# Kernel optimization log

Hardware: AMD Instinct MI355X
Metric: run time of the kernel (lower is better)

Reference implementation:

```python
import jax, jax.numpy as jnp
from jax import lax
import numpy as np

TEMPERATURE = 0.8
TOP_K = 50
TOP_P = 0.9
REP_PENALTY = 1.2


def setup_inputs() -> dict:
    key = jax.random.key(0)
    k1, k2 = jax.random.split(key)
    B, V, T = 256, 50257, 2048
    logits = jax.random.normal(k1, (B, V), dtype=jnp.float32) * 4.0  # spread so top-p is non-trivial
    generated = jax.random.randint(k2, (B, T), 0, V, dtype=jnp.int64)
    return {"logits": logits, "generated": generated}


def reference(logits, generated):
    """One decode-step of LLM.generate: temperature -> repetition penalty ->
    top-k filter -> top-p (nucleus) filter -> softmax -> multinomial sample.
    Returns (next_token [B], probs [B, V])."""
    B, V = logits.shape
    x = logits / TEMPERATURE

    # repetition penalty: divide logits at every previously-generated token id
    rows = jnp.arange(B)[:, None]
    present = jnp.zeros((B, V), dtype=bool).at[rows, generated].set(True)
    x = jnp.where(present, x / REP_PENALTY, x)

    # top-k: mask everything strictly below the k-th largest logit
    kth = lax.top_k(x, TOP_K)[0][:, -1:]  # [B, 1]
    x = jnp.where(x < kth, -jnp.inf, x)

    # top-p: sort descending, softmax, cumsum, drop tail mass > p (always keep top-1)
    order = jnp.argsort(-x, axis=-1)                      # [B, V] descending order
    sorted_logits = jnp.take_along_axis(x, order, axis=-1)
    cum = jnp.cumsum(jax.nn.softmax(sorted_logits, axis=-1), axis=-1)
    remove_sorted = (cum > TOP_P).at[:, 0].set(False)
    inv = jnp.argsort(order, axis=-1)                     # inverse permutation
    remove = jnp.take_along_axis(remove_sorted, inv, axis=-1)
    x = jnp.where(remove, -jnp.inf, x)

    probs = jax.nn.softmax(x, axis=-1)
    # multinomial sampling == categorical over the filtered logits
    next_token = jax.random.categorical(jax.random.key(42), x, axis=-1)  # [B]
    return next_token, probs
```

## Files before the change

### kernel.cpp

```cpp
#include <hip/hip_runtime.h>
#include <stdint.h>

#define V_CONST 50257
#define NMASK ((V_CONST + 31) / 32)
#define KTOP 50
#define CAND_CAP 1024
#define NTHREADS 1024
#define THR_SCREEN 13.0f
#define C_TEMP 1.25f
#define C_PEN ((float)(1.25 / 1.2))
#define THREEFRY_PARTITIONABLE 1

__device__ __forceinline__ void tf_round(uint32_t &x0, uint32_t &x1, int r) {
  x0 += x1;
  x1 = (x1 << r) | (x1 >> (32 - r));
  x1 ^= x0;
}

__device__ __forceinline__ uint2 threefry_k_0_42(uint32_t x0, uint32_t x1) {
  const uint32_t ks0 = 0u;
  const uint32_t ks1 = 42u;
  const uint32_t ks2 = 0x1BD11BDAu ^ 0u ^ 42u;
  x0 += ks0; x1 += ks1;
  tf_round(x0, x1, 13); tf_round(x0, x1, 15); tf_round(x0, x1, 26); tf_round(x0, x1, 6);
  x0 += ks1; x1 += ks2 + 1u;
  tf_round(x0, x1, 17); tf_round(x0, x1, 29); tf_round(x0, x1, 16); tf_round(x0, x1, 24);
  x0 += ks2; x1 += ks0 + 2u;
  tf_round(x0, x1, 13); tf_round(x0, x1, 15); tf_round(x0, x1, 26); tf_round(x0, x1, 6);
  x0 += ks0; x1 += ks1 + 3u;
  tf_round(x0, x1, 17); tf_round(x0, x1, 29); tf_round(x0, x1, 16); tf_round(x0, x1, 24);
  x0 += ks1; x1 += ks2 + 4u;
  tf_round(x0, x1, 13); tf_round(x0, x1, 15); tf_round(x0, x1, 26); tf_round(x0, x1, 6);
  x0 += ks2; x1 += ks0 + 5u;
  uint2 r; r.x = x0; r.y = x1; return r;
}

__device__ __forceinline__ float gumbel_at(uint32_t p, uint32_t half_total) {
  uint32_t bits;
#if THREEFRY_PARTITIONABLE
  uint2 o = threefry_k_0_42(0u, p);
  bits = o.x ^ o.y;
#else
  if (p < half_total) {
    uint2 o = threefry_k_0_42(p, p + half_total);
    bits = o.x;
  } else {
    uint2 o = threefry_k_0_42(p - half_total, p);
    bits = o.y;
  }
#endif
  uint32_t ub = (bits >> 9) | 0x3F800000u;
  float u = __uint_as_float(ub) - 1.0f;
  u = u + 1.17549435e-38f;
  u = fmaxf(1.17549435e-38f, u);
  return -logf(-logf(u));
}

__device__ __forceinline__ uint32_t f2u_desc(float f) {
  uint32_t b = __float_as_uint(f);
  return (b & 0x80000000u) ? ~b : (b | 0x80000000u);
}
__device__ __forceinline__ float u2f(uint32_t u) {
  uint32_t b = (u & 0x80000000u) ? (u & 0x7FFFFFFFu) : ~u;
  return __uint_as_float(b);
}

__global__ __launch_bounds__(NTHREADS) void sample_kernel(
    const float* __restrict__ logits, const int* __restrict__ generated,
    float* __restrict__ out, int B, int T) {
  const int b = blockIdx.x;
  const int tid = threadIdx.x;

  __shared__ uint32_t mask[NMASK];
  __shared__ uint32_t cu[CAND_CAP];
  __shared__ int      cidx[CAND_CAP];
  __shared__ uint32_t su[CAND_CAP];
  __shared__ int      sidx[CAND_CAP];
  __shared__ float    eg[CAND_CAP];
  __shared__ float    gg[CAND_CAP];
  __shared__ int s_cnt, s_nsurv, s_ovf, s_rlast;
  __shared__ float s_z2;

  for (int i = tid; i < NMASK; i += NTHREADS) mask[i] = 0u;
  if (tid == 0) s_cnt = 0;
  __syncthreads();

  const int* grow = generated + (size_t)b * T;
  int toks[4];
  int ntok = 0;
  for (int i = tid; i < T && ntok < 4; i += NTHREADS) toks[ntok++] = grow[i];

  const float* lrow = logits + (size_t)b * V_CONST;
  float* prow = out + B + (size_t)b * V_CONST;
  const int aoff = (4 - (b & 3)) & 3;
  const int tailn = (V_CONST - aoff) & 3;
  const int body4 = (V_CONST - aoff) >> 2;
  const float4* arow4 = (const float4*)(lrow + aoff);
  float4* orow4 = (float4*)(prow + aoff);
  const float4 z4 = make_float4(0.f, 0.f, 0.f, 0.f);

#define PUSH_RAW(xv, vv) do {                                          \
    int p_ = atomicAdd(&s_cnt, 1);                                     \
    if (p_ < CAND_CAP) { cu[p_] = __float_as_uint(xv); cidx[p_] = (vv); } \
  } while (0)

  {
    int t = tid;
    bool has = (t < body4);
    float4 rc;
    if (has) rc = arow4[t];
    while (has) {
      int t2 = t + NTHREADS;
      bool has2 = (t2 < body4);
      float4 rn;
      if (has2) rn = arow4[t2];
      orow4[t] = z4;
      int v0 = aoff + (t << 2);
      if (rc.x * C_TEMP >= THR_SCREEN) PUSH_RAW(rc.x, v0 + 0);
      if (rc.y * C_TEMP >= THR_SCREEN) PUSH_RAW(rc.y, v0 + 1);
      if (rc.z * C_TEMP >= THR_SCREEN) PUSH_RAW(rc.z, v0 + 2);
      if (rc.w * C_TEMP >= THR_SCREEN) PUSH_RAW(rc.w, v0 + 3);
      t = t2; rc = rn; has = has2;
    }
    if (tid < aoff + tailn) {
      int v = (tid < aoff) ? tid : (V_CONST - tailn) + (tid - aoff);
      prow[v] = 0.f;
      float x = lrow[v];
      if (x * C_TEMP >= THR_SCREEN) PUSH_RAW(x, v);
    }
  }
#undef PUSH_RAW

  for (int k = 0; k < ntok; k++) {
    int tok = toks[k];
    atomicOr(&mask[tok >> 5], 1u << (tok & 31));
  }
  for (int i = tid + 4 * NTHREADS; i < T; i += NTHREADS) {
    int tok = grow[i];
    atomicOr(&mask[tok >> 5], 1u << (tok & 31));
  }
  __syncthreads();

  const int total = s_cnt;
  int n = (total < CAND_CAP) ? total : CAND_CAP;
  bool ok = false;

  if (total >= KTOP && total <= CAND_CAP) {
    for (int i = tid; i < n; i += NTHREADS) {
      float x = __uint_as_float(cu[i]);
      int v = cidx[i];
      float xe = x / 0.8f;
      if ((mask[v >> 5] >> (v & 31)) & 1u) xe = xe / 1.2f;
      cu[i] = f2u_desc(xe);
    }
    __syncthreads();
    for (int i = tid; i < n; i += NTHREADS) {
      uint32_t ui = cu[i]; int ii = cidx[i];
      int rank = 0;
      for (int j = 0; j < n; j++) {
        uint32_t uj = cu[j];
        rank += ((uj > ui) || (uj == ui && cidx[j] < ii)) ? 1 : 0;
      }
      su[rank] = ui; sidx[rank] = ii;
    }
    __syncthreads();
    ok = (su[KTOP - 1] >= f2u_desc(THR_SCREEN) + 64u);
  }

  if (!ok) {
    float thr = THR_SCREEN;
    uint32_t ulo_ = 0u, uhi_ = 0xFFFFFFFFu;
    n = 0;
    for (int attempt = 0; attempt < 64; ++attempt) {
      __syncthreads();
      if (tid == 0) s_cnt = 0;
      __syncthreads();
      for (int t = tid; t < body4; t += NTHREADS) {
        float4 r = arow4[t];
        int v0 = aoff + (t << 2);
        uint32_t w = (mask[v0 >> 5] >> (v0 & 31)) & 0xFu;
        float m0 = (w & 1u) ? C_PEN : C_TEMP;
        float m1 = (w & 2u) ? C_PEN : C_TEMP;
        float m2 = (w & 4u) ? C_PEN : C_TEMP;
        float m3 = (w & 8u) ? C_PEN : C_TEMP;
        if (r.x * m0 >= thr) { int p = atomicAdd(&s_cnt, 1); if (p < CAND_CAP) { cu[p] = __float_as_uint(r.x); cidx[p] = v0; } }
        if (r.y * m1 >= thr) { int p = atomicAdd(&s_cnt, 1); if (p < CAND_CAP) { cu[p] = __float_as_uint(r.y); cidx[p] = v0 + 1; } }
        if (r.z * m2 >= thr) { int p = atomicAdd(&s_cnt, 1); if (p < CAND_CAP) { cu[p] = __float_as_uint(r.z); cidx[p] = v0 + 2; } }
        if (r.w * m3 >= thr) { int p = atomicAdd(&s_cnt, 1); if (p < CAND_CAP) { cu[p] = __float_as_uint(r.w); cidx[p] = v0 + 3; } }
      }
      if (tid < aoff + tailn) {
        int v = (tid < aoff) ? tid : (V_CONST - tailn) + (tid - aoff);
        float x = lrow[v];
        float m = ((mask[v >> 5] >> (v & 31)) & 1u) ? C_PEN : C_TEMP;
        if (x * m >= thr) { int p = atomicAdd(&s_cnt, 1); if (p < CAND_CAP) { cu[p] = __float_as_uint(x); cidx[p] = v; } }
      }
      __syncthreads();
      const int tot = s_cnt;
      n = (tot < CAND_CAP) ? tot : CAND_CAP;
      const bool window = (tot >= KTOP && tot <= CAND_CAP);
      const bool last = (attempt == 63);
      if (window || last) {
        if (n > 0) {
          for (int i = tid; i < n; i += NTHREADS) {
            float x = __uint_as_float(cu[i]);
            int v = cidx[i];
            float xe = x / 0.8f;
            if ((mask[v >> 5] >> (v & 31)) & 1u) xe = xe / 1.2f;
            cu[i] = f2u_desc(xe);
          }
          __syncthreads();
          for (int i = tid; i < n; i += NTHREADS) {
            uint32_t ui = cu[i]; int ii = cidx[i];
            int rank = 0;
            for (int j = 0; j < n; j++) {
              uint32_t uj = cu[j];
              rank += ((uj > ui) || (uj == ui && cidx[j] < ii)) ? 1 : 0;
            }
            su[rank] = ui; sidx[rank] = ii;
          }
          __syncthreads();
        }
        if (window) {
          if (su[KTOP - 1] >= f2u_desc(thr) + 64u) break;
          if (last) break;
          thr = u2f(su[KTOP - 1] >= 96u ? su[KTOP - 1] - 96u : 0u);
        } else break;
      } else if (tot < KTOP) {
        uhi_ = f2u_desc(thr);
        if (attempt == 0) thr = 11.0f;
        else {
          uint32_t mid = ulo_ + (uhi_ - ulo_) / 2u;
          if (mid >= uhi_) mid = uhi_ - 1u;
          thr = u2f(mid);
        }
      } else {
        ulo_ = f2u_desc(thr);
        uint32_t mid = ulo_ + (uhi_ - ulo_) / 2u;
        if (mid <= ulo_) mid = ulo_ + 1u;
        thr = u2f(mid);
      }
    }
  }

  if (n == 0) { if (tid == 0) out[b] = 0.f; return; }

  if (tid < 64) {
    int n64 = (n < 64) ? n : 64;
    uint32_t sur = (tid < n64) ? su[tid] : 0u;
    int kpos = (n < KTOP) ? (n - 1) : (KTOP - 1);
    uint32_t kth = __shfl(sur, kpos, 64);
    unsigned long long m = __ballot(tid < n64 && sur == kth);
    int hi = 63 - __clzll(m);
    if (tid == 0) {
      s_nsurv = hi + 1;
      s_ovf = (hi == n64 - 1 && n > n64) ? 1 : 0;
    }
  }
  __syncthreads();

  const uint32_t half_total = (uint32_t)((size_t)256 * V_CONST / 2);

  if (!s_ovf) {
    if (tid < 64) {
      const int nsurv = s_nsurv;
      uint32_t sur = (tid < nsurv) ? su[tid] : 0u;
      int sidr = (tid < nsurv) ? sidx[tid] : 0x7FFFFFFF;
      float f = u2f(sur);
      float s0 = __shfl(f, 0, 64);
      float egr = 0.f, ggr = 0.f;
      if (tid < nsurv) {
        egr = expf(f - s0);
        ggr = gumbel_at((uint32_t)(b * V_CONST + sidr), half_total);
      }
      float scr = f + ggr;
      float zall = 0.f;
      for (int j = 0; j < nsurv; j++) zall += __shfl(egr, j, 64);
      float cum = 0.f, z2 = 0.f;
      int rlast = 0;
      float best = -3.402823466e38f; int besti = V_CONST;
      for (int j = 0; j < nsurv; j++) {
        float e = __shfl(egr, j, 64);
        cum += e / zall;
        if (j == 0 || cum <= 0.9f) {
          rlast = j;
          z2 += e;
          float sc = __shfl(scr, j, 64);
          int idx = __shfl(sidr, j, 64);
          if (sc > best || (sc == best && idx < besti)) { best = sc; besti = idx; }
        } else break;
      }
      if (tid == 0) out[b] = (float)besti;
      if (tid <= rlast) prow[sidr] = egr / z2;
    }
    return;
  }

  {
    const int nsurv = s_nsurv;
    const float s0 = u2f(su[0]);
    for (int r = tid; r < nsurv; r += NTHREADS) {
      float f = u2f(su[r]);
      eg[r] = expf(f - s0);
      gg[r] = gumbel_at((uint32_t)(b * V_CONST + sidx[r]), half_total);
    }
    __syncthreads();
    if (tid == 0) {
      float zall = 0.f;
      for (int r = 0; r < nsurv; r++) zall += eg[r];
      float cum = 0.f;
      int rlast = 0;
      for (int r = 0; r < nsurv; r++) {
        cum += eg[r] / zall;
        if (r == 0 || cum <= 0.9f) rlast = r;
        else break;
      }
      float z2 = 0.f;
      for (int r = 0; r <= rlast; r++) z2 += eg[r];
      float best = -3.402823466e38f; int besti = V_CONST;
      for (int r = 0; r <= rlast; r++) {
        float sc = u2f(su[r]) + gg[r];
        int idx = sidx[r];
        if (sc > best || (sc == best && idx < besti)) { best = sc; besti = idx; }
      }
      out[b] = (float)besti;
      s_rlast = rlast; s_z2 = z2;
    }
    __syncthreads();
    const int rlast = s_rlast;
    const float z2 = s_z2;
    for (int r = tid; r <= rlast; r += NTHREADS) {
      prow[sidx[r]] = eg[r] / z2;
    }
  }
}

extern "C" void kernel_launch(void* const* d_in, const int* in_sizes, int n_in,
                              void* d_out, int out_size, void* d_ws, size_t ws_size,
                              hipStream_t stream) {
  const float* logits = (const float*)d_in[0];
  const int* generated = (const int*)d_in[1];
  float* out = (float*)d_out;
  const int B = in_sizes[0] / V_CONST;
  const int T = in_sizes[1] / B;
  hipLaunchKernelGGL(sample_kernel, dim3(B), dim3(NTHREADS), 0, stream,
                     logits, generated, out, B, T);
}
```

Baseline: 34.16 us.

## Split each row across four blocks with global candidate merge and last-block finalize

Each row is now screened by four 256-thread blocks, one per vocab quarter. Candidates go into a global per-row buffer through atomics, and a ticket counter picks the last-arriving block to zero the output row, rank-sort and sample. The aim is to fill more of the machine with 1024 smaller blocks instead of 256 big ones, and to build the presence mask before screening so the penalty is applied inline. In exchange it adds a memset launch, global atomics, a serialized zero-fill of the whole row by one 256-thread block, and a full mask rebuild on the fallback path.

```diff
diff --git a/kernel.cpp b/kernel.cpp
--- a/kernel.cpp
+++ b/kernel.cpp
@@ -5,10 +5,10 @@
 #define NMASK ((V_CONST + 31) / 32)
 #define KTOP 50
 #define CAND_CAP 1024
-#define NTHREADS 1024
 #define THR_SCREEN 13.0f
 #define C_TEMP 1.25f
 #define C_PEN ((float)(1.25 / 1.2))
+#define Q4L 12564
 #define THREEFRY_PARTITIONABLE 1
 
 __device__ __forceinline__ void tf_round(uint32_t &x0, uint32_t &x1, int r) {
@@ -65,185 +65,97 @@
   return __uint_as_float(b);
 }
 
-__global__ __launch_bounds__(NTHREADS) void sample_kernel(
-    const float* __restrict__ logits, const int* __restrict__ generated,
-    float* __restrict__ out, int B, int T) {
-  const int b = blockIdx.x;
-  const int tid = threadIdx.x;
-
-  __shared__ uint32_t mask[NMASK];
-  __shared__ uint32_t cu[CAND_CAP];
-  __shared__ int      cidx[CAND_CAP];
-  __shared__ uint32_t su[CAND_CAP];
-  __shared__ int      sidx[CAND_CAP];
-  __shared__ float    eg[CAND_CAP];
-  __shared__ float    gg[CAND_CAP];
-  __shared__ int s_cnt, s_nsurv, s_ovf, s_rlast;
-  __shared__ float s_z2;
-
-  for (int i = tid; i < NMASK; i += NTHREADS) mask[i] = 0u;
-  if (tid == 0) s_cnt = 0;
-  __syncthreads();
-
-  const int* grow = generated + (size_t)b * T;
-  int toks[4];
-  int ntok = 0;
-  for (int i = tid; i < T && ntok < 4; i += NTHREADS) toks[ntok++] = grow[i];
-
-  const float* lrow = logits + (size_t)b * V_CONST;
-  float* prow = out + B + (size_t)b * V_CONST;
-  const int aoff = (4 - (b & 3)) & 3;
-  const int tailn = (V_CONST - aoff) & 3;
-  const int body4 = (V_CONST - aoff) >> 2;
+template<int NT>
+__device__ __forceinline__ void rank_sort(int n, uint32_t* cu, int* cidx,
+                                          uint32_t* su, int* sidx, int tid) {
+  for (int i = tid; i < n; i += NT) {
+    uint32_t ui = cu[i]; int ii = cidx[i];
+    int rank = 0;
+    for (int j = 0; j < n; j++) {
+      uint32_t uj = cu[j];
+      rank += ((uj > ui) || (uj == ui && cidx[j] < ii)) ? 1 : 0;
+    }
+    su[rank] = ui; sidx[rank] = ii;
+  }
+}
+
+template<int NT>
+__device__ int rescan_bisect(const float* lrow, const uint32_t* mask,
+                             int aoff, int body4, int tailn,
+                             uint32_t* cu, int* cidx, uint32_t* su, int* sidx,
+                             int* s_cnt, int tid) {
   const float4* arow4 = (const float4*)(lrow + aoff);
-  float4* orow4 = (float4*)(prow + aoff);
-  const float4 z4 = make_float4(0.f, 0.f, 0.f, 0.f);
-
-#define PUSH_RAW(xv, vv) do {                                          \
-    int p_ = atomicAdd(&s_cnt, 1);                                     \
-    if (p_ < CAND_CAP) { cu[p_] = __float_as_uint(xv); cidx[p_] = (vv); } \
-  } while (0)
-
-  {
-    int t = tid;
-    bool has = (t < body4);
-    float4 rc;
-    if (has) rc = arow4[t];
-    while (has) {
-      int t2 = t + NTHREADS;
-      bool has2 = (t2 < body4);
-      float4 rn;
-      if (has2) rn = arow4[t2];
-      orow4[t] = z4;
+  float thr = THR_SCREEN;
+  uint32_t ulo_ = 0u, uhi_ = 0xFFFFFFFFu;
+  int n = 0;
+  for (int attempt = 0; attempt < 64; ++attempt) {
+    __syncthreads();
+    if (tid == 0) *s_cnt = 0;
+    __syncthreads();
+    for (int t = tid; t < body4; t += NT) {
+      float4 r = arow4[t];
       int v0 = aoff + (t << 2);
-      if (rc.x * C_TEMP >= THR_SCREEN) PUSH_RAW(rc.x, v0 + 0);
-      if (rc.y * C_TEMP >= THR_SCREEN) PUSH_RAW(rc.y, v0 + 1);
-      if (rc.z * C_TEMP >= THR_SCREEN) PUSH_RAW(rc.z, v0 + 2);
-      if (rc.w * C_TEMP >= THR_SCREEN) PUSH_RAW(rc.w, v0 + 3);
-      t = t2; rc = rn; has = has2;
+      uint32_t w = (mask[v0 >> 5] >> (v0 & 31)) & 0xFu;
+      float m0 = (w & 1u) ? C_PEN : C_TEMP;
+      float m1 = (w & 2u) ? C_PEN : C_TEMP;
+      float m2 = (w & 4u) ? C_PEN : C_TEMP;
+      float m3 = (w & 8u) ? C_PEN : C_TEMP;
+      if (r.x * m0 >= thr) { int p = atomicAdd(s_cnt, 1); if (p < CAND_CAP) { cu[p] = __float_as_uint(r.x); cidx[p] = v0; } }
+      if (r.y * m1 >= thr) { int p = atomicAdd(s_cnt, 1); if (p < CAND_CAP) { cu[p] = __float_as_uint(r.y); cidx[p] = v0 + 1; } }
+      if (r.z * m2 >= thr) { int p = atomicAdd(s_cnt, 1); if (p < CAND_CAP) { cu[p] = __float_as_uint(r.z); cidx[p] = v0 + 2; } }
+      if (r.w * m3 >= thr) { int p = atomicAdd(s_cnt, 1); if (p < CAND_CAP) { cu[p] = __float_as_uint(r.w); cidx[p] = v0 + 3; } }
     }
     if (tid < aoff + tailn) {
       int v = (tid < aoff) ? tid : (V_CONST - tailn) + (tid - aoff);
-      prow[v] = 0.f;
       float x = lrow[v];
-      if (x * C_TEMP >= THR_SCREEN) PUSH_RAW(x, v);
-    }
-  }
-#undef PUSH_RAW
-
-  for (int k = 0; k < ntok; k++) {
-    int tok = toks[k];
-    atomicOr(&mask[tok >> 5], 1u << (tok & 31));
-  }
-  for (int i = tid + 4 * NTHREADS; i < T; i += NTHREADS) {
-    int tok = grow[i];
-    atomicOr(&mask[tok >> 5], 1u << (tok & 31));
-  }
-  __syncthreads();
-
-  const int total = s_cnt;
-  int n = (total < CAND_CAP) ? total : CAND_CAP;
-  bool ok = false;
-
-  if (total >= KTOP && total <= CAND_CAP) {
-    for (int i = tid; i < n; i += NTHREADS) {
-      float x = __uint_as_float(cu[i]);
-      int v = cidx[i];
-      float xe = x / 0.8f;
-      if ((mask[v >> 5] >> (v & 31)) & 1u) xe = xe / 1.2f;
-      cu[i] = f2u_desc(xe);
-    }
-    __syncthreads();
-    for (int i = tid; i < n; i += NTHREADS) {
-      uint32_t ui = cu[i]; int ii = cidx[i];
-      int rank = 0;
-      for (int j = 0; j < n; j++) {
-        uint32_t uj = cu[j];
-        rank += ((uj > ui) || (uj == ui && cidx[j] < ii)) ? 1 : 0;
-      }
-      su[rank] = ui; sidx[rank] = ii;
-    }
-    __syncthreads();
-    ok = (su[KTOP - 1] >= f2u_desc(THR_SCREEN) + 64u);
-  }
-
-  if (!ok) {
-    float thr = THR_SCREEN;
-    uint32_t ulo_ = 0u, uhi_ = 0xFFFFFFFFu;
-    n = 0;
-    for (int attempt = 0; attempt < 64; ++attempt) {
-      __syncthreads();
-      if (tid == 0) s_cnt = 0;
-      __syncthreads();
-      for (int t = tid; t < body4; t += NTHREADS) {
-        float4 r = arow4[t];
-        int v0 = aoff + (t << 2);
-        uint32_t w = (mask[v0 >> 5] >> (v0 & 31)) & 0xFu;
-        float m0 = (w & 1u) ? C_PEN : C_TEMP;
-        float m1 = (w & 2u) ? C_PEN : C_TEMP;
-        float m2 = (w & 4u) ? C_PEN : C_TEMP;
-        float m3 = (w & 8u) ? C_PEN : C_TEMP;
-        if (r.x * m0 >= thr) { int p = atomicAdd(&s_cnt, 1); if (p < CAND_CAP) { cu[p] = __float_as_uint(r.x); cidx[p] = v0; } }
-        if (r.y * m1 >= thr) { int p = atomicAdd(&s_cnt, 1); if (p < CAND_CAP) { cu[p] = __float_as_uint(r.y); cidx[p] = v0 + 1; } }
-        if (r.z * m2 >= thr) { int p = atomicAdd(&s_cnt, 1); if (p < CAND_CAP) { cu[p] = __float_as_uint(r.z); cidx[p] = v0 + 2; } }
-        if (r.w * m3 >= thr) { int p = atomicAdd(&s_cnt, 1); if (p < CAND_CAP) { cu[p] = __float_as_uint(r.w); cidx[p] = v0 + 3; } }
-      }
-      if (tid < aoff + tailn) {
-        int v = (tid < aoff) ? tid : (V_CONST - tailn) + (tid - aoff);
-        float x = lrow[v];
-        float m = ((mask[v >> 5] >> (v & 31)) & 1u) ? C_PEN : C_TEMP;
-        if (x * m >= thr) { int p = atomicAdd(&s_cnt, 1); if (p < CAND_CAP) { cu[p] = __float_as_uint(x); cidx[p] = v; } }
-      }
-      __syncthreads();
-      const int tot = s_cnt;
-      n = (tot < CAND_CAP) ? tot : CAND_CAP;
-      const bool window = (tot >= KTOP && tot <= CAND_CAP);
-      const bool last = (attempt == 63);
-      if (window || last) {
-        if (n > 0) {
-          for (int i = tid; i < n; i += NTHREADS) {
-            float x = __uint_as_float(cu[i]);
-            int v = cidx[i];
-            float xe = x / 0.8f;
-            if ((mask[v >> 5] >> (v & 31)) & 1u) xe = xe / 1.2f;
-            cu[i] = f2u_desc(xe);
-          }
-          __syncthreads();
-          for (int i = tid; i < n; i += NTHREADS) {
-            uint32_t ui = cu[i]; int ii = cidx[i];
-            int rank = 0;
-            for (int j = 0; j < n; j++) {
-              uint32_t uj = cu[j];
-              rank += ((uj > ui) || (uj == ui && cidx[j] < ii)) ? 1 : 0;
-            }
-            su[rank] = ui; sidx[rank] = ii;
-          }
-          __syncthreads();
+      float m = ((mask[v >> 5] >> (v & 31)) & 1u) ? C_PEN : C_TEMP;
+      if (x * m >= thr) { int p = atomicAdd(s_cnt, 1); if (p < CAND_CAP) { cu[p] = __float_as_uint(x); cidx[p] = v; } }
+    }
+    __syncthreads();
+    const int tot = *s_cnt;
+    n = (tot < CAND_CAP) ? tot : CAND_CAP;
+    const bool window = (tot >= KTOP && tot <= CAND_CAP);
+    const bool last = (attempt == 63);
+    if (window || last) {
+      if (n > 0) {
+        for (int i = tid; i < n; i += NT) {
+          float x = __uint_as_float(cu[i]);
+          int v = cidx[i];
+          float xe = x / 0.8f;
+          if ((mask[v >> 5] >> (v & 31)) & 1u) xe = xe / 1.2f;
+          cu[i] = f2u_desc(xe);
         }
-        if (window) {
-          if (su[KTOP - 1] >= f2u_desc(thr) + 64u) break;
-          if (last) break;
-          thr = u2f(su[KTOP - 1] >= 96u ? su[KTOP - 1] - 96u : 0u);
-        } else break;
-      } else if (tot < KTOP) {
-        uhi_ = f2u_desc(thr);
-        if (attempt == 0) thr = 11.0f;
-        else {
-          uint32_t mid = ulo_ + (uhi_ - ulo_) / 2u;
-          if (mid >= uhi_) mid = uhi_ - 1u;
-          thr = u2f(mid);
-        }
-      } else {
-        ulo_ = f2u_desc(thr);
+        __syncthreads();
+        rank_sort<NT>(n, cu, cidx, su, sidx, tid);
+        __syncthreads();
+      }
+      if (window) {
+        if (su[KTOP - 1] >= f2u_desc(thr) + 64u) break;
+        if (last) break;
+        thr = u2f(su[KTOP - 1] >= 96u ? su[KTOP - 1] - 96u : 0u);
+      } else break;
+    } else if (tot < KTOP) {
+      uhi_ = f2u_desc(thr);
+      if (attempt == 0) thr = 11.0f;
+      else {
         uint32_t mid = ulo_ + (uhi_ - ulo_) / 2u;
-        if (mid <= ulo_) mid = ulo_ + 1u;
+        if (mid >= uhi_) mid = uhi_ - 1u;
         thr = u2f(mid);
       }
-    }
-  }
-
-  if (n == 0) { if (tid == 0) out[b] = 0.f; return; }
-
+    } else {
+      ulo_ = f2u_desc(thr);
+      uint32_t mid = ulo_ + (uhi_ - ulo_) / 2u;
+      if (mid <= ulo_) mid = ulo_ + 1u;
+      thr = u2f(mid);
+    }
+  }
+  return n;
+}
+
+template<int NT>
+__device__ void sample_tail(int n, uint32_t* su, int* sidx, float* eg, float* gg,
+                            float* out, float* prow, int b, int B, int tid,
+                            int* s_nsurv, int* s_ovf, int* s_rlast, float* s_z2) {
   if (tid < 64) {
     int n64 = (n < 64) ? n : 64;
     uint32_t sur = (tid < n64) ? su[tid] : 0u;
@@ -251,18 +163,13 @@
     uint32_t kth = __shfl(sur, kpos, 64);
     unsigned long long m = __ballot(tid < n64 && sur == kth);
     int hi = 63 - __clzll(m);
-    if (tid == 0) {
-      s_nsurv = hi + 1;
-      s_ovf = (hi == n64 - 1 && n > n64) ? 1 : 0;
-    }
-  }
-  __syncthreads();
-
-  const uint32_t half_total = (uint32_t)((size_t)256 * V_CONST / 2);
-
-  if (!s_ovf) {
+    if (tid == 0) { *s_nsurv = hi + 1; *s_ovf = (hi == n64 - 1 && n > n64) ? 1 : 0; }
+  }
+  __syncthreads();
+  const uint32_t half_total = (uint32_t)((size_t)B * V_CONST / 2);
+  if (!(*s_ovf)) {
     if (tid < 64) {
-      const int nsurv = s_nsurv;
+      const int nsurv = *s_nsurv;
       uint32_t sur = (tid < nsurv) ? su[tid] : 0u;
       int sidr = (tid < nsurv) ? sidx[tid] : 0x7FFFFFFF;
       float f = u2f(sur);
@@ -282,23 +189,21 @@
         float e = __shfl(egr, j, 64);
         cum += e / zall;
         if (j == 0 || cum <= 0.9f) {
-          rlast = j;
-          z2 += e;
+          rlast = j; z2 += e;
           float sc = __shfl(scr, j, 64);
           int idx = __shfl(sidr, j, 64);
           if (sc > best || (sc == best && idx < besti)) { best = sc; besti = idx; }
         } else break;
       }
       if (tid == 0) out[b] = (float)besti;
-      if (tid <= rlast) prow[sidr] = egr / z2;
+      if (tid <= rlast && tid < nsurv) prow[sidr] = egr / z2;
     }
     return;
   }
-
   {
-    const int nsurv = s_nsurv;
+    const int nsurv = *s_nsurv;
     const float s0 = u2f(su[0]);
-    for (int r = tid; r < nsurv; r += NTHREADS) {
+    for (int r = tid; r < nsurv; r += NT) {
       float f = u2f(su[r]);
       eg[r] = expf(f - s0);
       gg[r] = gumbel_at((uint32_t)(b * V_CONST + sidx[r]), half_total);
@@ -307,8 +212,7 @@
     if (tid == 0) {
       float zall = 0.f;
       for (int r = 0; r < nsurv; r++) zall += eg[r];
-      float cum = 0.f;
-      int rlast = 0;
+      float cum = 0.f; int rlast = 0;
       for (int r = 0; r < nsurv; r++) {
         cum += eg[r] / zall;
         if (r == 0 || cum <= 0.9f) rlast = r;
@@ -323,15 +227,214 @@
         if (sc > best || (sc == best && idx < besti)) { best = sc; besti = idx; }
       }
       out[b] = (float)besti;
-      s_rlast = rlast; s_z2 = z2;
-    }
-    __syncthreads();
-    const int rlast = s_rlast;
-    const float z2 = s_z2;
-    for (int r = tid; r <= rlast; r += NTHREADS) {
-      prow[sidx[r]] = eg[r] / z2;
-    }
-  }
+      *s_rlast = rlast; *s_z2 = z2;
+    }
+    __syncthreads();
+    const int rlast = *s_rlast;
+    const float z2 = *s_z2;
+    for (int r = tid; r <= rlast; r += NT) prow[sidx[r]] = eg[r] / z2;
+  }
+}
+
+#define QNT 256
+__global__ __launch_bounds__(QNT) void quad_kernel(
+    const float* __restrict__ logits, const int* __restrict__ generated,
+    float* __restrict__ out, unsigned int* __restrict__ tickets,
+    unsigned int* __restrict__ rowcnt, unsigned long long* __restrict__ pairs,
+    int B, int T) {
+  const int bid = blockIdx.x;
+  const int b = bid >> 2, q = bid & 3;
+  const int tid = threadIdx.x;
+  const int vlo = q * Q4L;
+  const int len = (q == 3) ? (V_CONST - 3 * Q4L) : Q4L;
+  const int vhi = vlo + len;
+  const int w0 = vlo >> 5;
+  const int nw = ((vhi + 31) >> 5) - w0;
+
+  __shared__ uint32_t mask[NMASK];
+  __shared__ uint32_t cu[CAND_CAP];
+  __shared__ int      cidx[CAND_CAP];
+  __shared__ uint32_t su[CAND_CAP];
+  __shared__ int      sidx[CAND_CAP];
+  __shared__ int s_cnt, s_win, s_nsurv, s_ovf, s_rlast;
+  __shared__ float s_z2;
+  float* eg = (float*)cu;
+  float* gg = (float*)cidx;
+
+  for (int i = tid; i < nw; i += QNT) mask[i] = 0u;
+  __syncthreads();
+
+  const int* grow = generated + (size_t)b * T;
+  for (int i = tid; i < T; i += QNT) {
+    int tok = grow[i];
+    if (tok >= vlo && tok < vhi)
+      atomicOr(&mask[(tok >> 5) - w0], 1u << (tok & 31));
+  }
+  __syncthreads();
+
+  const float* lrow = logits + (size_t)b * V_CONST;
+  float* prow = out + B + (size_t)b * V_CONST;
+  const int aoff = (4 - (b & 3)) & 3;
+  const int body4 = (len - aoff) >> 2;
+  const int tailn = (len - aoff) & 3;
+  const float4* arow4 = (const float4*)(lrow + vlo + aoff);
+  unsigned long long* rowpairs = pairs + (size_t)b * CAND_CAP;
+
+#define SCREEN1(xv, vv) do {                                              \
+    int v_ = (vv); float x_ = (xv);                                       \
+    if (x_ * C_TEMP >= THR_SCREEN) {                                      \
+      uint32_t pres_ = (mask[(v_ >> 5) - w0] >> (v_ & 31)) & 1u;          \
+      float xe_ = x_ / 0.8f; if (pres_) xe_ = xe_ / 1.2f;                 \
+      unsigned int slot_ = atomicAdd(&rowcnt[b], 1u);                     \
+      if (slot_ < CAND_CAP)                                               \
+        atomicExch(&rowpairs[slot_],                                      \
+                   ((unsigned long long)f2u_desc(xe_) << 32) | (uint32_t)v_); \
+    } } while (0)
+
+  for (int t = tid; t < body4; t += QNT) {
+    float4 r = arow4[t];
+    int v0 = vlo + aoff + (t << 2);
+    SCREEN1(r.x, v0 + 0);
+    SCREEN1(r.y, v0 + 1);
+    SCREEN1(r.z, v0 + 2);
+    SCREEN1(r.w, v0 + 3);
+  }
+  if (tid < aoff + tailn) {
+    int v = (tid < aoff) ? (vlo + tid) : (vhi - tailn + (tid - aoff));
+    SCREEN1(lrow[v], v);
+  }
+#undef SCREEN1
+
+  __syncthreads();
+  if (tid == 0) s_win = (atomicAdd(&tickets[b], 1u) == 3u) ? 1 : 0;
+  __syncthreads();
+  if (!s_win) return;
+
+  {
+    const int ftailn = (V_CONST - aoff) & 3;
+    const int fbody4 = (V_CONST - aoff) >> 2;
+    float4* orow4 = (float4*)(prow + aoff);
+    const float4 z4 = make_float4(0.f, 0.f, 0.f, 0.f);
+    for (int t = tid; t < fbody4; t += QNT) orow4[t] = z4;
+    if (tid < aoff + ftailn) {
+      int v = (tid < aoff) ? tid : (V_CONST - ftailn) + (tid - aoff);
+      prow[v] = 0.f;
+    }
+  }
+
+  if (tid == 0) s_cnt = (int)atomicAdd(&rowcnt[b], 0u);
+  __syncthreads();
+  const int total = s_cnt;
+  int n = (total < CAND_CAP) ? total : CAND_CAP;
+  bool ok = false;
+
+  if (total >= KTOP && total <= CAND_CAP) {
+    for (int i = tid; i < n; i += QNT) {
+      unsigned long long pr = atomicAdd(&rowpairs[i], 0ull);
+      cu[i] = (uint32_t)(pr >> 32);
+      cidx[i] = (int)(uint32_t)pr;
+    }
+    __syncthreads();
+    rank_sort<QNT>(n, cu, cidx, su, sidx, tid);
+    __syncthreads();
+    ok = (su[KTOP - 1] >= f2u_desc(THR_SCREEN) + 64u);
+  }
+
+  if (!ok) {
+    for (int i = tid; i < NMASK; i += QNT) mask[i] = 0u;
+    __syncthreads();
+    for (int i = tid; i < T; i += QNT) {
+      int tok = grow[i];
+      atomicOr(&mask[tok >> 5], 1u << (tok & 31));
+    }
+    const int ftailn = (V_CONST - aoff) & 3;
+    const int fbody4 = (V_CONST - aoff) >> 2;
+    n = rescan_bisect<QNT>(lrow, mask, aoff, fbody4, ftailn,
+                           cu, cidx, su, sidx, &s_cnt, tid);
+  }
+
+  if (n == 0) { if (tid == 0) out[b] = 0.f; return; }
+  sample_tail<QNT>(n, su, sidx, eg, gg, out, prow, b, B, tid,
+                   &s_nsurv, &s_ovf, &s_rlast, &s_z2);
+}
+
+#define MNT 1024
+__global__ __launch_bounds__(MNT) void mono_kernel(
+    const float* __restrict__ logits, const int* __restrict__ generated,
+    float* __restrict__ out, int B, int T) {
+  const int b = blockIdx.x;
+  const int tid = threadIdx.x;
+  __shared__ uint32_t mask[NMASK];
+  __shared__ uint32_t cu[CAND_CAP];
+  __shared__ int      cidx[CAND_CAP];
+  __shared__ uint32_t su[CAND_CAP];
+  __shared__ int      sidx[CAND_CAP];
+  __shared__ int s_cnt, s_nsurv, s_ovf, s_rlast;
+  __shared__ float s_z2;
+  float* eg = (float*)cu;
+  float* gg = (float*)cidx;
+
+  for (int i = tid; i < NMASK; i += MNT) mask[i] = 0u;
+  if (tid == 0) s_cnt = 0;
+  __syncthreads();
+  const int* grow = generated + (size_t)b * T;
+  for (int i = tid; i < T; i += MNT) {
+    int tok = grow[i];
+    atomicOr(&mask[tok >> 5], 1u << (tok & 31));
+  }
+  __syncthreads();
+
+  const float* lrow = logits + (size_t)b * V_CONST;
+  float* prow = out + B + (size_t)b * V_CONST;
+  const int aoff = (4 - (b & 3)) & 3;
+  const int tailn = (V_CONST - aoff) & 3;
+  const int body4 = (V_CONST - aoff) >> 2;
+  const float4* arow4 = (const float4*)(lrow + aoff);
+  float4* orow4 = (float4*)(prow + aoff);
+  const float4 z4 = make_float4(0.f, 0.f, 0.f, 0.f);
+
+#define SCREEN1(xv, vv) do {                                          \
+    int v_ = (vv); float x_ = (xv);                                   \
+    if (x_ * C_TEMP >= THR_SCREEN) {                                  \
+      uint32_t pres_ = (mask[v_ >> 5] >> (v_ & 31)) & 1u;             \
+      float xe_ = x_ / 0.8f; if (pres_) xe_ = xe_ / 1.2f;             \
+      int p_ = atomicAdd(&s_cnt, 1);                                  \
+      if (p_ < CAND_CAP) { cu[p_] = f2u_desc(xe_); cidx[p_] = v_; }   \
+    } } while (0)
+  for (int t = tid; t < body4; t += MNT) {
+    float4 r = arow4[t];
+    orow4[t] = z4;
+    int v0 = aoff + (t << 2);
+    SCREEN1(r.x, v0 + 0);
+    SCREEN1(r.y, v0 + 1);
+    SCREEN1(r.z, v0 + 2);
+    SCREEN1(r.w, v0 + 3);
+  }
+  if (tid < aoff + tailn) {
+    int v = (tid < aoff) ? tid : (V_CONST - tailn) + (tid - aoff);
+    prow[v] = 0.f;
+    SCREEN1(lrow[v], v);
+  }
+#undef SCREEN1
+  __syncthreads();
+
+  const int total = s_cnt;
+  int n = (total < CAND_CAP) ? total : CAND_CAP;
+  bool ok = false;
+  if (total >= KTOP && total <= CAND_CAP) {
+    rank_sort<MNT>(n, cu, cidx, su, sidx, tid);
+    __syncthreads();
+    ok = (su[KTOP - 1] >= f2u_desc(THR_SCREEN) + 64u);
+  } else {
+    __syncthreads();
+  }
+  if (!ok) {
+    n = rescan_bisect<MNT>(lrow, mask, aoff, body4, tailn,
+                           cu, cidx, su, sidx, &s_cnt, tid);
+  }
+  if (n == 0) { if (tid == 0) out[b] = 0.f; return; }
+  sample_tail<MNT>(n, su, sidx, eg, gg, out, prow, b, B, tid,
+                   &s_nsurv, &s_ovf, &s_rlast, &s_z2);
 }
 
 extern "C" void kernel_launch(void* const* d_in, const int* in_sizes, int n_in,
@@ -342,6 +445,18 @@
   float* out = (float*)d_out;
   const int B = in_sizes[0] / V_CONST;
   const int T = in_sizes[1] / B;
-  hipLaunchKernelGGL(sample_kernel, dim3(B), dim3(NTHREADS), 0, stream,
-                     logits, generated, out, B, T);
-}
+
+  const size_t pairs_off = 8192;
+  const size_t needed = pairs_off + (size_t)B * CAND_CAP * sizeof(unsigned long long);
+  if (ws_size >= needed && B <= 1024) {
+    unsigned int* tickets = (unsigned int*)d_ws;
+    unsigned int* rowcnt = (unsigned int*)((char*)d_ws + 4096);
+    unsigned long long* pairs = (unsigned long long*)((char*)d_ws + pairs_off);
+    hipMemsetAsync(d_ws, 0, 8192, stream);
+    hipLaunchKernelGGL(quad_kernel, dim3(4 * B), dim3(QNT), 0, stream,
+                       logits, generated, out, tickets, rowcnt, pairs, B, T);
+  } else {
+    hipLaunchKernelGGL(mono_kernel, dim3(B), dim3(MNT), 0, stream,
+                       logits, generated, out, B, T);
+  }
+}
```

Measured after the change: 112.6 us. +229.5%, slower.
